# Performance work log

Hardware: AMD Instinct MI355X
Metric: run time of the kernel (lower is better)

Reference implementation:

```python
import jax, jax.numpy as jnp
import numpy as np

N, E, G = 50000, 1600000, 64
N_SPECIES, D_ATTR, D, N_RBF = 16, 16, 32, 8
CUTOFF = 5.0
SCALE, SHIFT = 1.0, 0.0


def setup_inputs() -> dict:
    key = jax.random.key(0)
    ks = jax.random.split(key, 20)

    def w(k, shape):
        fan_in = shape[-2] if len(shape) > 1 else shape[-1]
        return jax.random.normal(k, shape, dtype=jnp.float32) / np.sqrt(fan_in)

    return {
        "x": jax.random.randint(ks[0], (N, 1), 0, N_SPECIES),
        "pos": 3.0 * jax.random.normal(ks[1], (N, 3), dtype=jnp.float32),
        "edge_index": jax.random.randint(ks[2], (2, E), 0, N),
        "period_vec": 0.1 * jax.random.normal(ks[3], (E, 3), dtype=jnp.float32),
        "batch": jnp.sort(jax.random.randint(ks[4], (N,), 0, G)),
        "W_elem": w(ks[5], (N_SPECIES, D_ATTR)),
        "W0": w(ks[6], (D_ATTR, D)),
        "b0": jnp.zeros((D,), jnp.float32),
        "Wr1": w(ks[7], (3, N_RBF, D)),
        "br1": jnp.zeros((3, D), jnp.float32),
        "Wr2": w(ks[8], (3, D, D)),
        "Wmsg": w(ks[9], (3, D, D)),
        "Wattr": w(ks[10], (3, D_ATTR, D)),
        "Wself": w(ks[11], (3, D, D)),
        "bconv": jnp.zeros((3, D), jnp.float32),
        "wsh": w(ks[12], (3, 4)),
        "Wp1": w(ks[13], (D, 16)),
        "bp1": jnp.zeros((16,), jnp.float32),
        "Wp2": w(ks[14], (16, 1)),
        "bp2": jnp.zeros((1,), jnp.float32),
    }


def reference(x, pos, edge_index, period_vec, batch, W_elem, W0, b0, Wr1, br1,
              Wr2, Wmsg, Wattr, Wself, bconv, wsh, Wp1, bp1, Wp2, bp2):
    src, dst = edge_index[0], edge_index[1]

    # node_attr_layer: species embedding (gather), then first_atom_embed linear
    x_attr = W_elem[x[:, 0]]                              # [N, D_ATTR]
    h = x_attr @ W0 + b0                                  # [N, D]

    # edge_attr_layer: PBC edge vectors, lengths, l<=1 spherical harmonics
    edge_vec = pos[dst] - pos[src] + period_vec           # [E, 3]
    edge_len = jnp.linalg.norm(edge_vec, axis=-1, keepdims=True)  # [E, 1]
    unit = edge_vec / (edge_len + 1e-9)
    edge_sh = jnp.concatenate([jnp.ones_like(edge_len), unit], axis=-1)  # [E, 4]

    # edge_embedding_layer: Gaussian radial basis of edge lengths
    centers = jnp.linspace(0.0, CUTOFF, N_RBF, dtype=pos.dtype)
    gamma = jnp.asarray((N_RBF / CUTOFF) ** 2, pos.dtype)
    rbf = jnp.exp(-gamma * (edge_len - centers) ** 2)     # [E, N_RBF]

    # 3 conv layers: gather -> per-edge transform -> scatter-sum -> node update
    for i in range(3):
        rw = jax.nn.relu(rbf @ Wr1[i] + br1[i]) @ Wr2[i]  # [E, D] radial MLP
        sh_w = edge_sh @ wsh[i]                           # [E] sh mixing
        msg = (h[src] @ Wmsg[i]) * rw * sh_w[:, None]     # [E, D]
        agg = jax.ops.segment_sum(msg, dst, num_segments=N)  # [N, D]
        h = jax.nn.silu(agg + x_attr @ Wattr[i] + h @ Wself[i] + bconv[i])

    # post_conv layers
    h = jax.nn.silu(h @ Wp1 + bp1)                        # [N, 16]
    h = (h @ Wp2 + bp2)[:, 0]                             # [N] (squeeze)

    # scatter-sum pooling over graphs + affine energy scaling
    e = jax.ops.segment_sum(h, batch, num_segments=G)     # [G]
    return (e * SCALE + SHIFT)[:, None]                   # [G, 1]
```

## Files before the change

kernel.cpp:

```cpp
#include <hip/hip_runtime.h>
#include <hip/hip_fp16.h>
#include <math.h>

constexpr int N_NODES  = 50000;
constexpr int N_EDGES  = 1600000;
constexpr int G_GRAPHS = 64;
constexpr int D        = 32;
constexpr int D_ATTR   = 16;
constexpr int N_RBF    = 8;

constexpr int   TBL      = 8192;
constexpr int   TBL_ROWS = TBL + 1;
constexpr float LMAX     = 10.0f;

constexpr int BUCKET = 80;

constexpr int NT     = 64;
constexpr int NTILES = (N_NODES + NT - 1) / NT;
constexpr int TCAP   = 2432;
constexpr int EPB    = 8192;
constexpr int NBLK1  = (N_EDGES + EPB - 1) / EPB;

typedef unsigned int uint4v __attribute__((ext_vector_type(4)));

__device__ __forceinline__ float silu(float x) {
    return x / (1.0f + __expf(-x));
}
__device__ __forceinline__ float h2f_lo(unsigned int w) {
    return __half2float(__ushort_as_half((unsigned short)(w & 0xFFFF)));
}
__device__ __forceinline__ float h2f_hi(unsigned int w) {
    return __half2float(__ushort_as_half((unsigned short)(w >> 16)));
}

__global__ void node_init_kernel(const int* __restrict__ x,
                                 const float* __restrict__ W_elem,
                                 const float* __restrict__ W0,
                                 const float* __restrict__ b0,
                                 const float* __restrict__ Wmsg0,
                                 const float* __restrict__ Wself0,
                                 const float* __restrict__ Wattr,
                                 const float* __restrict__ bconv,
                                 __half* __restrict__ hm0,
                                 float* __restrict__ hs0,
                                 float* __restrict__ xa1,
                                 float* __restrict__ xa2) {
    int t = blockIdx.x * blockDim.x + threadIdx.x;
    int n = t >> 5, c = t & 31;
    if (n >= N_NODES) return;
    int sp = x[n];
    const float* we = W_elem + sp * D_ATTR;
    float xv = (c < D_ATTR) ? we[c] : 0.0f;
    float acc = b0[c];
#pragma unroll
    for (int a = 0; a < D_ATTR; ++a) acc += we[a] * W0[a * D + c];
    float m = 0.0f, s = 0.0f;
#pragma unroll
    for (int j = 0; j < D; ++j) {
        float hj = __shfl(acc, j, 32);
        m = fmaf(hj, Wmsg0[j * D + c], m);
        s = fmaf(hj, Wself0[j * D + c], s);
    }
    float a0 = bconv[0 * D + c], a1 = bconv[1 * D + c], a2 = bconv[2 * D + c];
#pragma unroll
    for (int j = 0; j < D_ATTR; ++j) {
        float xj = __shfl(xv, j, 32);
        a0 = fmaf(xj, Wattr[0 * D_ATTR * D + j * D + c], a0);
        a1 = fmaf(xj, Wattr[1 * D_ATTR * D + j * D + c], a1);
        a2 = fmaf(xj, Wattr[2 * D_ATTR * D + j * D + c], a2);
    }
    hm0[n * D + c] = __float2half(m);
    hs0[n * D + c] = s + a0;
    xa1[n * D + c] = a1;
    xa2[n * D + c] = a2;
}

__global__ __launch_bounds__(256) void scatter_kernel(const int* __restrict__ eidx,
                                                      const float* __restrict__ pos,
                                                      const float* __restrict__ period,
                                                      const float* __restrict__ wsh,
                                                      int* __restrict__ tile_cursor,
                                                      uint4v* __restrict__ bins) {
    __shared__ int hist[NTILES];
    __shared__ int basev[NTILES];
    int tid = threadIdx.x;
    int e0 = blockIdx.x * EPB;
    for (int i = tid; i < NTILES; i += 256) hist[i] = 0;
    __syncthreads();
#pragma unroll 4
    for (int i = 0; i < EPB / 256; ++i) {
        int e = e0 + tid + 256 * i;
        if (e < N_EDGES) atomicAdd(&hist[eidx[N_EDGES + e] >> 6], 1);
    }
    __syncthreads();
    for (int t = tid; t < NTILES; t += 256) {
        int cnt = hist[t];
        basev[t] = (cnt > 0) ? atomicAdd(&tile_cursor[t], cnt) : 0;
        hist[t] = 0;
    }
    __syncthreads();
    for (int i = 0; i < EPB / 256; ++i) {
        int e = e0 + tid + 256 * i;
        if (e >= N_EDGES) continue;
        int s = eidx[e];
        int d = eidx[N_EDGES + e];
        float vx = pos[d * 3 + 0] - pos[s * 3 + 0] + period[e * 3 + 0];
        float vy = pos[d * 3 + 1] - pos[s * 3 + 1] + period[e * 3 + 1];
        float vz = pos[d * 3 + 2] - pos[s * 3 + 2] + period[e * 3 + 2];
        float len = sqrtf(vx * vx + vy * vy + vz * vz);
        float inv = 1.0f / (len + 1e-9f);
        int idx = (int)fminf(len * ((float)TBL / LMAX) + 0.5f, (float)TBL);
        float sw[3];
#pragma unroll
        for (int l = 0; l < 3; ++l)
            sw[l] = wsh[l * 4 + 0] + (vx * wsh[l * 4 + 1] + vy * wsh[l * 4 + 2] + vz * wsh[l * 4 + 3]) * inv;
        int tile = d >> 6;
        int rank = atomicAdd(&hist[tile], 1);
        int slot = basev[tile] + rank;
        if (slot < TCAP) {
            unsigned u0 = (unsigned)__half_as_ushort(__float2half(sw[0]));
            unsigned u1 = (unsigned)__half_as_ushort(__float2half(sw[1]));
            unsigned u2 = (unsigned)__half_as_ushort(__float2half(sw[2]));
            uint4v r;
            r.x = (unsigned)s | ((unsigned)idx << 16);
            r.y = (unsigned)(d & (NT - 1));
            r.z = u0 | (u1 << 16);
            r.w = u2;
            bins[(size_t)tile * TCAP + slot] = r;
        }
    }
}

__global__ __launch_bounds__(256) void shuffle_kernel(const uint4v* __restrict__ bins,
                                                      const int* __restrict__ tile_cursor,
                                                      uint4v* __restrict__ rec,
                                                      int* __restrict__ count) {
    __shared__ int lcur[NT];
    int tile = blockIdx.x;
    int tid = threadIdx.x;
    if (tid < NT) lcur[tid] = 0;
    __syncthreads();
    int cnt = tile_cursor[tile];
    if (cnt > TCAP) cnt = TCAP;
    const uint4v* base = bins + (size_t)tile * TCAP;
    for (int i = tid; i < cnt; i += 256) {
        uint4v r = __builtin_nontemporal_load(base + i);
        int dl = (int)r.y;
        int slot = atomicAdd(&lcur[dl], 1);
        if (slot < BUCKET) {
            uint4v o;
            o.x = r.x; o.y = r.z; o.z = r.w; o.w = 0u;
            rec[(size_t)(tile * NT + dl) * BUCKET + slot] = o;
        }
    }
    __syncthreads();
    if (tid < NT) {
        int node = tile * NT + tid;
        if (node < N_NODES) {
            int c = lcur[tid];
            count[node] = c < BUCKET ? c : BUCKET;
        }
    }
}

__global__ void table_kernel(const float* __restrict__ Wr1,
                             const float* __restrict__ br1,
                             const float* __restrict__ Wr2,
                             __half* __restrict__ table) {
    int t = blockIdx.x * blockDim.x + threadIdx.x;
    if (t >= 3 * TBL_ROWS) return;
    int l = t / TBL_ROWS;
    int idx = t % TBL_ROWS;
    float len = (float)idx * (LMAX / (float)TBL);
    const float gamma = (8.0f / 5.0f) * (8.0f / 5.0f);
    float rbf[N_RBF];
#pragma unroll
    for (int k = 0; k < N_RBF; ++k) {
        float dd = len - (float)k * (5.0f / 7.0f);
        rbf[k] = __expf(-gamma * dd * dd);
    }
    float out[D];
#pragma unroll
    for (int c = 0; c < D; ++c) out[c] = 0.0f;
    for (int j = 0; j < D; ++j) {
        float z = br1[l * D + j];
#pragma unroll
        for (int k = 0; k < N_RBF; ++k) z += rbf[k] * Wr1[l * N_RBF * D + k * D + j];
        z = fmaxf(z, 0.0f);
        const float* w2 = Wr2 + l * D * D + j * D;
#pragma unroll
        for (int c = 0; c < D; ++c) out[c] += z * w2[c];
    }
    __half* dst = table + ((size_t)(l * TBL_ROWS + idx)) * D;
#pragma unroll
    for (int c = 0; c < D; ++c) dst[c] = __float2half(out[c]);
}

template <int LAYER, bool NEXT>
__global__ void conv_kernel(const __half* __restrict__ hm,
                            const float* __restrict__ hs,
                            const uint4v* __restrict__ rec,
                            const int* __restrict__ count,
                            const __half* __restrict__ table,
                            const float* __restrict__ Wmsg_next,
                            const float* __restrict__ Wself_next,
                            const float* __restrict__ xa_next,
                            __half* __restrict__ hm_out,
                            float* __restrict__ hs_out,
                            float* __restrict__ h_final) {
    int gtid = blockIdx.x * blockDim.x + threadIdx.x;
    int node = gtid >> 6;
    if (node >= N_NODES) return;
    int lane = threadIdx.x & 63;
    int qw = lane >> 4;
    int q  = lane & 15;

    const __half2* tab2 = (const __half2*)(table + ((size_t)LAYER * TBL_ROWS) * D);
    const __half2* hm2  = (const __half2*)hm;
    int cnt = count[node];
    int beg = node * BUCKET;

    float ax = 0.0f, ay = 0.0f;
    if (cnt > 0) {
        int end = beg + cnt;
        int last = end - 1;
        for (int base = beg + qw; base < end; base += 32) {
            uint4v r[8];
#pragma unroll
            for (int j = 0; j < 8; ++j) {
                int slot = base + 4 * j;
                r[j] = __builtin_nontemporal_load(rec + (slot <= last ? slot : last));
            }
#pragma unroll
            for (int j = 0; j < 8; ++j) {
                int slot = base + 4 * j;
                int s = (int)(r[j].x & 0xFFFFu);
                int i = (int)(r[j].x >> 16);
                float sw = (LAYER == 0) ? h2f_lo(r[j].y)
                         : (LAYER == 1) ? h2f_hi(r[j].y)
                                        : h2f_lo(r[j].z);
                sw = (slot <= last) ? sw : 0.0f;
                float2 tf = __half22float2(tab2[i * 16 + q]);
                float2 mf = __half22float2(hm2[s * 16 + q]);
                ax = fmaf(tf.x * mf.x, sw, ax);
                ay = fmaf(tf.y * mf.y, sw, ay);
            }
        }
    }
    ax += __shfl_xor(ax, 16);
    ax += __shfl_xor(ax, 32);
    ay += __shfl_xor(ay, 16);
    ay += __shfl_xor(ay, 32);

    int c = lane & 31;
    float vx = __shfl(ax, c >> 1);
    float vy = __shfl(ay, c >> 1);
    float agg = (c & 1) ? vy : vx;

    if ((lane >> 5) == 0) {
        float hn = silu(agg + hs[node * D + c]);
        if (NEXT) {
            float m = 0.0f, s2 = 0.0f;
#pragma unroll
            for (int j = 0; j < D; ++j) {
                float hj = __shfl(hn, j);
                m  = fmaf(hj, Wmsg_next[j * D + c], m);
                s2 = fmaf(hj, Wself_next[j * D + c], s2);
            }
            hm_out[node * D + c] = __float2half(m);
            hs_out[node * D + c] = s2 + xa_next[node * D + c];
        } else {
            h_final[node * D + c] = hn;
        }
    }
}

__global__ void readout_kernel(const float* __restrict__ h,
                               const int* __restrict__ batch,
                               const float* __restrict__ Wp1,
                               const float* __restrict__ bp1,
                               const float* __restrict__ Wp2,
                               const float* __restrict__ bp2,
                               float* __restrict__ out) {
    int n = blockIdx.x * blockDim.x + threadIdx.x;
    float s = 0.0f;
    int b = -1;
    if (n < N_NODES) {
        b = batch[n];
        const float* hrow = h + n * D;
        float acc2 = bp2[0];
#pragma unroll
        for (int m = 0; m < 16; ++m) {
            float a = bp1[m];
#pragma unroll
            for (int j = 0; j < D; ++j) a += hrow[j] * Wp1[j * 16 + m];
            acc2 += silu(a) * Wp2[m];
        }
        s = acc2;
    }
    unsigned long long valid = __ballot(n < N_NODES);
    if (valid == 0ull) return;
    int firstLane = __ffsll(valid) - 1;
    int b0v = __shfl(b, firstLane);
    bool ok = (b == b0v) || (n >= N_NODES);
    if (__all(ok)) {
#pragma unroll
        for (int o = 32; o > 0; o >>= 1) s += __shfl_down(s, o);
        if ((threadIdx.x & 63) == 0) atomicAdd(out + b0v, s);
    } else {
        if (n < N_NODES) atomicAdd(out + b, s);
    }
}

extern "C" void kernel_launch(void* const* d_in, const int* in_sizes, int n_in,
                              void* d_out, int out_size, void* d_ws, size_t ws_size,
                              hipStream_t stream) {
    const int*   x      = (const int*)d_in[0];
    const float* pos    = (const float*)d_in[1];
    const int*   eidx   = (const int*)d_in[2];
    const float* period = (const float*)d_in[3];
    const int*   batch  = (const int*)d_in[4];
    const float* W_elem = (const float*)d_in[5];
    const float* W0     = (const float*)d_in[6];
    const float* b0     = (const float*)d_in[7];
    const float* Wr1    = (const float*)d_in[8];
    const float* br1    = (const float*)d_in[9];
    const float* Wr2    = (const float*)d_in[10];
    const float* Wmsg   = (const float*)d_in[11];
    const float* Wattr  = (const float*)d_in[12];
    const float* Wself  = (const float*)d_in[13];
    const float* bconv  = (const float*)d_in[14];
    const float* wsh    = (const float*)d_in[15];
    const float* Wp1    = (const float*)d_in[16];
    const float* bp1    = (const float*)d_in[17];
    const float* Wp2    = (const float*)d_in[18];
    const float* bp2    = (const float*)d_in[19];

    char* base = (char*)d_ws;
    size_t off = 0;
    auto carve = [&](size_t bytes) -> void* {
        void* p = base + off;
        off = (off + bytes + 255) & ~(size_t)255;
        return p;
    };
    __half* hm_a        = (__half*)carve((size_t)N_NODES * D * 2);
    __half* hm_b        = (__half*)carve((size_t)N_NODES * D * 2);
    float*  hs_a        = (float*)carve((size_t)N_NODES * D * 4);
    float*  hs_b        = (float*)carve((size_t)N_NODES * D * 4);
    float*  xa1         = (float*)carve((size_t)N_NODES * D * 4);
    float*  xa2         = (float*)carve((size_t)N_NODES * D * 4);
    float*  h_final     = (float*)carve((size_t)N_NODES * D * 4);
    uint4v* rec         = (uint4v*)carve((size_t)NTILES * NT * BUCKET * 16);
    uint4v* bins        = (uint4v*)carve((size_t)NTILES * TCAP * 16);
    int*    tile_cursor = (int*)carve((size_t)NTILES * 4);
    int*    count       = (int*)carve((size_t)NTILES * NT * 4);
    __half* table       = (__half*)carve((size_t)3 * TBL_ROWS * D * 2);
    (void)ws_size; (void)in_sizes; (void)n_in; (void)out_size;

    hipMemsetAsync(tile_cursor, 0, (size_t)NTILES * 4, stream);
    hipMemsetAsync(d_out, 0, (size_t)G_GRAPHS * 4, stream);

    node_init_kernel<<<(N_NODES * 32 + 255) / 256, 256, 0, stream>>>(
        x, W_elem, W0, b0, Wmsg + 0 * D * D, Wself + 0 * D * D, Wattr, bconv,
        hm_a, hs_a, xa1, xa2);
    scatter_kernel<<<NBLK1, 256, 0, stream>>>(eidx, pos, period, wsh, tile_cursor, bins);
    table_kernel<<<(3 * TBL_ROWS + 127) / 128, 128, 0, stream>>>(Wr1, br1, Wr2, table);
    shuffle_kernel<<<NTILES, 256, 0, stream>>>(bins, tile_cursor, rec, count);

    int cgrid = (N_NODES * 64 + 255) / 256;
    conv_kernel<0, true><<<cgrid, 256, 0, stream>>>(
        hm_a, hs_a, rec, count, table, Wmsg + 1 * D * D, Wself + 1 * D * D, xa1,
        hm_b, hs_b, nullptr);
    conv_kernel<1, true><<<cgrid, 256, 0, stream>>>(
        hm_b, hs_b, rec, count, table, Wmsg + 2 * D * D, Wself + 2 * D * D, xa2,
        hm_a, hs_a, nullptr);
    conv_kernel<2, false><<<cgrid, 256, 0, stream>>>(
        hm_a, hs_a, rec, count, table, nullptr, nullptr, nullptr,
        nullptr, nullptr, h_final);

    readout_kernel<<<(N_NODES + 255) / 256, 256, 0, stream>>>(h_final, batch, Wp1, bp1, Wp2, bp2,
                                                              (float*)d_out);
}
```

Measured before the change: 423.3 us.

## Split edge records into SoA arrays and vectorize per-lane loads in conv

Replaces the 16-byte AoS edge records with separate arrays: a 4-byte packed src/table-index word plus per-layer fp16 sh weights. Each conv layer now reads only 6 bytes per edge instead of 16, and each lane loads 4 consecutive slots at once with vector loads. The scatter bins are also split into three SoA arrays, and edges per scatter block are halved. The risk is more store instructions in scatter and shuffle, plus possible reads past a node's bucket end that are masked but still touch memory.

```diff
diff --git a/kernel.cpp b/kernel.cpp
--- a/kernel.cpp
+++ b/kernel.cpp
@@ -18,19 +18,19 @@
 constexpr int NT     = 64;
 constexpr int NTILES = (N_NODES + NT - 1) / NT;
 constexpr int TCAP   = 2432;
-constexpr int EPB    = 8192;
+constexpr int EPB    = 4096;
 constexpr int NBLK1  = (N_EDGES + EPB - 1) / EPB;
 
-typedef unsigned int uint4v __attribute__((ext_vector_type(4)));
+constexpr int NSLOT = NTILES * NT * BUCKET;
+
+typedef unsigned int  uint4v  __attribute__((ext_vector_type(4)));
+typedef unsigned int  uint2v  __attribute__((ext_vector_type(2)));
 
 __device__ __forceinline__ float silu(float x) {
     return x / (1.0f + __expf(-x));
 }
-__device__ __forceinline__ float h2f_lo(unsigned int w) {
-    return __half2float(__ushort_as_half((unsigned short)(w & 0xFFFF)));
-}
-__device__ __forceinline__ float h2f_hi(unsigned int w) {
-    return __half2float(__ushort_as_half((unsigned short)(w >> 16)));
+__device__ __forceinline__ float h2f_bits(unsigned short u) {
+    return __half2float(__ushort_as_half(u));
 }
 
 __global__ void node_init_kernel(const int* __restrict__ x,
@@ -80,7 +80,9 @@
                                                       const float* __restrict__ period,
                                                       const float* __restrict__ wsh,
                                                       int* __restrict__ tile_cursor,
-                                                      uint4v* __restrict__ bins) {
+                                                      unsigned int* __restrict__ binx,
+                                                      unsigned int* __restrict__ biny,
+                                                      unsigned int* __restrict__ binz) {
     __shared__ int hist[NTILES];
     __shared__ int basev[NTILES];
     int tid = threadIdx.x;
@@ -121,19 +123,20 @@
             unsigned u0 = (unsigned)__half_as_ushort(__float2half(sw[0]));
             unsigned u1 = (unsigned)__half_as_ushort(__float2half(sw[1]));
             unsigned u2 = (unsigned)__half_as_ushort(__float2half(sw[2]));
-            uint4v r;
-            r.x = (unsigned)s | ((unsigned)idx << 16);
-            r.y = (unsigned)(d & (NT - 1));
-            r.z = u0 | (u1 << 16);
-            r.w = u2;
-            bins[(size_t)tile * TCAP + slot] = r;
-        }
-    }
-}
-
-__global__ __launch_bounds__(256) void shuffle_kernel(const uint4v* __restrict__ bins,
+            size_t g = (size_t)tile * TCAP + slot;
+            binx[g] = (unsigned)s | ((unsigned)idx << 16);
+            biny[g] = u0 | (u1 << 16);
+            binz[g] = (unsigned)(d & (NT - 1)) | (u2 << 16);
+        }
+    }
+}
+
+__global__ __launch_bounds__(256) void shuffle_kernel(const unsigned int* __restrict__ binx,
+                                                      const unsigned int* __restrict__ biny,
+                                                      const unsigned int* __restrict__ binz,
                                                       const int* __restrict__ tile_cursor,
-                                                      uint4v* __restrict__ rec,
+                                                      unsigned int* __restrict__ xs,
+                                                      unsigned short* __restrict__ swp,
                                                       int* __restrict__ count) {
     __shared__ int lcur[NT];
     int tile = blockIdx.x;
@@ -142,15 +145,19 @@
     __syncthreads();
     int cnt = tile_cursor[tile];
     if (cnt > TCAP) cnt = TCAP;
-    const uint4v* base = bins + (size_t)tile * TCAP;
+    size_t base = (size_t)tile * TCAP;
     for (int i = tid; i < cnt; i += 256) {
-        uint4v r = __builtin_nontemporal_load(base + i);
-        int dl = (int)r.y;
+        unsigned rx = __builtin_nontemporal_load(binx + base + i);
+        unsigned ry = __builtin_nontemporal_load(biny + base + i);
+        unsigned rz = __builtin_nontemporal_load(binz + base + i);
+        int dl = (int)(rz & 63u);
         int slot = atomicAdd(&lcur[dl], 1);
         if (slot < BUCKET) {
-            uint4v o;
-            o.x = r.x; o.y = r.z; o.z = r.w; o.w = 0u;
-            rec[(size_t)(tile * NT + dl) * BUCKET + slot] = o;
+            size_t g = (size_t)(tile * NT + dl) * BUCKET + slot;
+            xs[g] = rx;
+            swp[0 * (size_t)NSLOT + g] = (unsigned short)(ry & 0xFFFFu);
+            swp[1 * (size_t)NSLOT + g] = (unsigned short)(ry >> 16);
+            swp[2 * (size_t)NSLOT + g] = (unsigned short)(rz >> 16);
         }
     }
     __syncthreads();
@@ -199,7 +206,8 @@
 template <int LAYER, bool NEXT>
 __global__ void conv_kernel(const __half* __restrict__ hm,
                             const float* __restrict__ hs,
-                            const uint4v* __restrict__ rec,
+                            const unsigned int* __restrict__ xs,
+                            const unsigned short* __restrict__ swp,
                             const int* __restrict__ count,
                             const __half* __restrict__ table,
                             const float* __restrict__ Wmsg_next,
@@ -217,34 +225,39 @@
 
     const __half2* tab2 = (const __half2*)(table + ((size_t)LAYER * TBL_ROWS) * D);
     const __half2* hm2  = (const __half2*)hm;
+    const unsigned short* swb = swp + (size_t)LAYER * NSLOT;
     int cnt = count[node];
     int beg = node * BUCKET;
+    int end = beg + cnt;
 
     float ax = 0.0f, ay = 0.0f;
-    if (cnt > 0) {
-        int end = beg + cnt;
-        int last = end - 1;
-        for (int base = beg + qw; base < end; base += 32) {
-            uint4v r[8];
-#pragma unroll
-            for (int j = 0; j < 8; ++j) {
-                int slot = base + 4 * j;
-                r[j] = __builtin_nontemporal_load(rec + (slot <= last ? slot : last));
-            }
-#pragma unroll
-            for (int j = 0; j < 8; ++j) {
-                int slot = base + 4 * j;
-                int s = (int)(r[j].x & 0xFFFFu);
-                int i = (int)(r[j].x >> 16);
-                float sw = (LAYER == 0) ? h2f_lo(r[j].y)
-                         : (LAYER == 1) ? h2f_hi(r[j].y)
-                                        : h2f_lo(r[j].z);
-                sw = (slot <= last) ? sw : 0.0f;
-                float2 tf = __half22float2(tab2[i * 16 + q]);
-                float2 mf = __half22float2(hm2[s * 16 + q]);
-                ax = fmaf(tf.x * mf.x, sw, ax);
-                ay = fmaf(tf.y * mf.y, sw, ay);
-            }
+    for (int base = beg; base < end; base += 32) {
+        int o0 = base + qw * 4;
+        int o1 = o0 + 16;
+        uint4v x0 = __builtin_nontemporal_load((const uint4v*)(xs + o0));
+        uint4v x1 = __builtin_nontemporal_load((const uint4v*)(xs + o1));
+        uint2v w0 = __builtin_nontemporal_load((const uint2v*)(swb + o0));
+        uint2v w1 = __builtin_nontemporal_load((const uint2v*)(swb + o1));
+        unsigned u[8];
+        unsigned short wv[8];
+        u[0] = x0.x; u[1] = x0.y; u[2] = x0.z; u[3] = x0.w;
+        u[4] = x1.x; u[5] = x1.y; u[6] = x1.z; u[7] = x1.w;
+        wv[0] = (unsigned short)(w0.x & 0xFFFFu); wv[1] = (unsigned short)(w0.x >> 16);
+        wv[2] = (unsigned short)(w0.y & 0xFFFFu); wv[3] = (unsigned short)(w0.y >> 16);
+        wv[4] = (unsigned short)(w1.x & 0xFFFFu); wv[5] = (unsigned short)(w1.x >> 16);
+        wv[6] = (unsigned short)(w1.y & 0xFFFFu); wv[7] = (unsigned short)(w1.y >> 16);
+#pragma unroll
+        for (int j = 0; j < 8; ++j) {
+            int slot = (j < 4) ? (o0 + j) : (o1 + j - 4);
+            bool valid = slot < end;
+            unsigned uu = valid ? u[j] : 0u;
+            float sw = valid ? h2f_bits(wv[j]) : 0.0f;
+            int s = (int)(uu & 0xFFFFu);
+            int i = (int)(uu >> 16);
+            float2 tf = __half22float2(tab2[i * 16 + q]);
+            float2 mf = __half22float2(hm2[s * 16 + q]);
+            ax = fmaf(tf.x * mf.x, sw, ax);
+            ay = fmaf(tf.y * mf.y, sw, ay);
         }
     }
     ax += __shfl_xor(ax, 16);
@@ -343,18 +356,21 @@
         off = (off + bytes + 255) & ~(size_t)255;
         return p;
     };
-    __half* hm_a        = (__half*)carve((size_t)N_NODES * D * 2);
-    __half* hm_b        = (__half*)carve((size_t)N_NODES * D * 2);
-    float*  hs_a        = (float*)carve((size_t)N_NODES * D * 4);
-    float*  hs_b        = (float*)carve((size_t)N_NODES * D * 4);
-    float*  xa1         = (float*)carve((size_t)N_NODES * D * 4);
-    float*  xa2         = (float*)carve((size_t)N_NODES * D * 4);
-    float*  h_final     = (float*)carve((size_t)N_NODES * D * 4);
-    uint4v* rec         = (uint4v*)carve((size_t)NTILES * NT * BUCKET * 16);
-    uint4v* bins        = (uint4v*)carve((size_t)NTILES * TCAP * 16);
-    int*    tile_cursor = (int*)carve((size_t)NTILES * 4);
-    int*    count       = (int*)carve((size_t)NTILES * NT * 4);
-    __half* table       = (__half*)carve((size_t)3 * TBL_ROWS * D * 2);
+    __half*         hm_a        = (__half*)carve((size_t)N_NODES * D * 2);
+    __half*         hm_b        = (__half*)carve((size_t)N_NODES * D * 2);
+    float*          hs_a        = (float*)carve((size_t)N_NODES * D * 4);
+    float*          hs_b        = (float*)carve((size_t)N_NODES * D * 4);
+    float*          xa1         = (float*)carve((size_t)N_NODES * D * 4);
+    float*          xa2         = (float*)carve((size_t)N_NODES * D * 4);
+    float*          h_final     = (float*)carve((size_t)N_NODES * D * 4);
+    unsigned int*   xs          = (unsigned int*)carve((size_t)NSLOT * 4);
+    unsigned short* swp         = (unsigned short*)carve((size_t)3 * NSLOT * 2);
+    unsigned int*   binx        = (unsigned int*)carve((size_t)NTILES * TCAP * 4);
+    unsigned int*   biny        = (unsigned int*)carve((size_t)NTILES * TCAP * 4);
+    unsigned int*   binz        = (unsigned int*)carve((size_t)NTILES * TCAP * 4);
+    int*            tile_cursor = (int*)carve((size_t)NTILES * 4);
+    int*            count       = (int*)carve((size_t)NTILES * NT * 4);
+    __half*         table       = (__half*)carve((size_t)3 * TBL_ROWS * D * 2);
     (void)ws_size; (void)in_sizes; (void)n_in; (void)out_size;
 
     hipMemsetAsync(tile_cursor, 0, (size_t)NTILES * 4, stream);
@@ -363,19 +379,20 @@
     node_init_kernel<<<(N_NODES * 32 + 255) / 256, 256, 0, stream>>>(
         x, W_elem, W0, b0, Wmsg + 0 * D * D, Wself + 0 * D * D, Wattr, bconv,
         hm_a, hs_a, xa1, xa2);
-    scatter_kernel<<<NBLK1, 256, 0, stream>>>(eidx, pos, period, wsh, tile_cursor, bins);
+    scatter_kernel<<<NBLK1, 256, 0, stream>>>(eidx, pos, period, wsh, tile_cursor,
+                                              binx, biny, binz);
     table_kernel<<<(3 * TBL_ROWS + 127) / 128, 128, 0, stream>>>(Wr1, br1, Wr2, table);
-    shuffle_kernel<<<NTILES, 256, 0, stream>>>(bins, tile_cursor, rec, count);
+    shuffle_kernel<<<NTILES, 256, 0, stream>>>(binx, biny, binz, tile_cursor, xs, swp, count);
 
     int cgrid = (N_NODES * 64 + 255) / 256;
     conv_kernel<0, true><<<cgrid, 256, 0, stream>>>(
-        hm_a, hs_a, rec, count, table, Wmsg + 1 * D * D, Wself + 1 * D * D, xa1,
+        hm_a, hs_a, xs, swp, count, table, Wmsg + 1 * D * D, Wself + 1 * D * D, xa1,
         hm_b, hs_b, nullptr);
     conv_kernel<1, true><<<cgrid, 256, 0, stream>>>(
-        hm_b, hs_b, rec, count, table, Wmsg + 2 * D * D, Wself + 2 * D * D, xa2,
+        hm_b, hs_b, xs, swp, count, table, Wmsg + 2 * D * D, Wself + 2 * D * D, xa2,
         hm_a, hs_a, nullptr);
     conv_kernel<2, false><<<cgrid, 256, 0, stream>>>(
-        hm_a, hs_a, rec, count, table, nullptr, nullptr, nullptr,
+        hm_a, hs_a, xs, swp, count, table, nullptr, nullptr, nullptr,
         nullptr, nullptr, h_final);
 
     readout_kernel<<<(N_NODES + 255) / 256, 256, 0, stream>>>(h_final, batch, Wp1, bp1, Wp2, bp2,
```

After: 452.0 us. 1.07x slower.
